# Optimization experiments

Hardware: AMD Instinct MI355X
Metric: run time of the kernel (lower is better)

Reference implementation:

```python
import jax, jax.numpy as jnp
import numpy as np

TOP_K = 2


def setup_inputs() -> dict:
    key = jax.random.key(0)
    k1, k2, k3, k4 = jax.random.split(key, 4)
    B, T, D = 1, 2048, 1024
    E, F = 8, 2048
    scale_in = 1.0 / np.sqrt(D)
    scale_f = 1.0 / np.sqrt(F)
    x = jax.random.normal(k1, (B, T, D), dtype=jnp.float32)
    Wr = jax.random.normal(k2, (E, D), dtype=jnp.float32) * scale_in  # router weight [E, D]
    W1 = jax.random.normal(k3, (E, F, D), dtype=jnp.float32) * scale_in  # fc1 weights stacked [E, F, D]
    W2 = jax.random.normal(k4, (E, D, F), dtype=jnp.float32) * scale_f  # fc2 weights stacked [E, D, F]
    return {"x": x, "Wr": Wr, "W1": W1, "W2": W2}


def reference(x, Wr, W1, W2):
    B, T, D = x.shape
    E = Wr.shape[0]
    xf = x.reshape(B * T, D)  # [N, D]
    N = xf.shape[0]

    # Router: softmax over experts, top-k gating, renormalized
    logits = xf @ Wr.T  # [N, E]
    probs = jax.nn.softmax(logits, axis=-1)
    top_vals, top_idx = jax.lax.top_k(probs, TOP_K)  # [N, K]
    top_vals = top_vals / jnp.sum(top_vals, axis=-1, keepdims=True)

    # Dense per-token gate matrix: gates[n, e] = sum_k top_vals[n,k] * (top_idx[n,k]==e)
    gates = jnp.zeros((N, E), dtype=x.dtype).at[
        jnp.arange(N)[:, None], top_idx
    ].add(top_vals)  # [N, E]

    # Expert MLP: fc2(relu(fc1(x))^2), computed densely for all experts then
    # combined with the (mostly-zero) gate weights.
    h = jnp.einsum("nd,efd->nef", xf, W1)  # [N, E, F]
    a = jnp.square(jax.nn.relu(h))
    y = jnp.einsum("nef,edf->ned", a, W2)  # [N, E, D]
    out = jnp.einsum("ne,ned->nd", gates, y)  # [N, D]
    return out.reshape(B, T, D)
```

## Files before the change

kernel.cpp:

```cpp
#include <hip/hip_runtime.h>
#include <hip/hip_bf16.h>
#include <cstdint>
#include <cstddef>

#define N_TOK 2048
#define DIM   1024
#define NEXP  8
#define FDIM  2048

#define BM 128
#define BN 128
#define BK 64

typedef __attribute__((ext_vector_type(8))) short short8;
typedef __attribute__((ext_vector_type(4))) float f32x4;
typedef unsigned short ushort_t;

#define OFF_COUNTS  0
#define OFF_TOK     4096
#define OFF_GATE    (OFF_TOK + NEXP * N_TOK * 4)
#define OFF_A       ((size_t)1 << 20)
#define OFF_W1B     (OFF_A  + (size_t)2 * N_TOK * FDIM * 2)
#define OFF_W2B     (OFF_W1B + (size_t)NEXP * FDIM * DIM * 2)
#define OFF_XB      (OFF_W2B + (size_t)NEXP * DIM * FDIM * 2)

__device__ __forceinline__ uint32_t cvt2(float lo, float hi) {
  __hip_bfloat162 p = __float22bfloat162_rn(make_float2(lo, hi));
  uint32_t r; __builtin_memcpy(&r, &p, 4); return r;
}

__device__ __forceinline__ void gl16(const ushort_t* g, const ushort_t* l) {
  __builtin_amdgcn_global_load_lds(
      (const __attribute__((address_space(1))) void*)g,
      (__attribute__((address_space(3))) void*)l, 16, 0, 0);
}

#define W1_U8 ((size_t)NEXP * FDIM * DIM / 8)
#define W2_U8 W1_U8
#define X_U8  ((size_t)N_TOK * DIM / 8)
__global__ __launch_bounds__(256) void prep_kernel(
    const float* __restrict__ W1, const float* __restrict__ W2, const float* __restrict__ x,
    ushort_t* __restrict__ W1b, ushort_t* __restrict__ W2b, ushort_t* __restrict__ xb) {
  size_t stride = (size_t)gridDim.x * 256;
  for (size_t u = (size_t)blockIdx.x * 256 + threadIdx.x; u < W1_U8 + W2_U8 + X_U8; u += stride) {
    const float* s; ushort_t* d; size_t o;
    if (u < W1_U8)              { s = W1; d = W1b; o = u; }
    else if (u < W1_U8 + W2_U8) { s = W2; d = W2b; o = u - W1_U8; }
    else                        { s = x;  d = xb;  o = u - W1_U8 - W2_U8; }
    float4 a = *(const float4*)(s + o * 8);
    float4 b = *(const float4*)(s + o * 8 + 4);
    *(uint4*)(d + o * 8) = make_uint4(cvt2(a.x, a.y), cvt2(a.z, a.w), cvt2(b.x, b.y), cvt2(b.z, b.w));
  }
}

__global__ __launch_bounds__(64) void router_kernel(
    const float* __restrict__ x, const float* __restrict__ Wr,
    int* __restrict__ counts, int* __restrict__ toklist,
    float* __restrict__ gatelist) {
  int n = blockIdx.x;
  int lane = threadIdx.x;
  const float* xr = x + (size_t)n * DIM;

  float xv[DIM / 64];
#pragma unroll
  for (int i = 0; i < DIM / 64; ++i) xv[i] = xr[lane + 64 * i];

  float logit[NEXP];
#pragma unroll
  for (int e = 0; e < NEXP; ++e) {
    const float* wr = Wr + (size_t)e * DIM;
    float s = 0.f;
#pragma unroll
    for (int i = 0; i < DIM / 64; ++i) s += xv[i] * wr[lane + 64 * i];
#pragma unroll
    for (int off = 32; off; off >>= 1) s += __shfl_down(s, off);
    logit[e] = s;
  }

  if (lane == 0) {
    float m = logit[0];
#pragma unroll
    for (int e = 1; e < NEXP; ++e) m = fmaxf(m, logit[e]);
    float p[NEXP];
#pragma unroll
    for (int e = 0; e < NEXP; ++e) p[e] = expf(logit[e] - m);
    int i1 = 0;
#pragma unroll
    for (int e = 1; e < NEXP; ++e) if (p[e] > p[i1]) i1 = e;
    int i2 = (i1 == 0) ? 1 : 0;
#pragma unroll
    for (int e = 0; e < NEXP; ++e)
      if (e != i1 && p[e] > p[i2]) i2 = e;
    float denom = p[i1] + p[i2];

    int pos1 = atomicAdd(&counts[i1], 1);
    toklist[i1 * N_TOK + pos1] = n;
    gatelist[i1 * N_TOK + pos1] = p[i1] / denom;

    int pos2 = atomicAdd(&counts[i2], 1);
    toklist[i2 * N_TOK + pos2] = n;
    gatelist[i2 * N_TOK + pos2] = p[i2] / denom;
  }
}

__global__ __launch_bounds__(256, 3) void fc1_mfma(
    const ushort_t* __restrict__ xb, const ushort_t* __restrict__ W1b,
    const int* __restrict__ counts, const int* __restrict__ toklist,
    __hip_bfloat16* __restrict__ Abuf) {
  const int ROWB = N_TOK / BM;
  const int COLB = FDIM / BN;
  int bid = blockIdx.x;
  int e  = bid / (ROWB * COLB);
  int rb = (bid / COLB) % ROWB;
  int cb = bid % COLB;
  int ne = counts[e];
  if (rb * BM >= ne) return;
  int base = 0;
  for (int i = 0; i < e; ++i) base += counts[i];

  __shared__ ushort_t As[BM * BK];
  __shared__ ushort_t Bs[BN * BK];

  int tid = threadIdx.x, lane = tid & 63, w = tid >> 6;

  const ushort_t* gA[4]; const ushort_t* gB[4];
  const ushort_t* lA[4]; const ushort_t* lB[4];
#pragma unroll
  for (int i = 0; i < 4; ++i) {
    int row = w * 32 + i * 8 + (lane >> 3);
    int c16 = (lane & 7) ^ (row & 7);
    int r = rb * BM + row; if (r >= ne) r = ne - 1;
    int tok = toklist[e * N_TOK + r];
    gA[i] = xb + (size_t)tok * DIM + c16 * 8;
    gB[i] = W1b + ((size_t)e * FDIM + cb * BN + row) * DIM + c16 * 8;
    lA[i] = &As[w * 2048 + i * 512];
    lB[i] = &Bs[w * 2048 + i * 512];
  }

  int wr = (w >> 1) * 64, wc = (w & 1) * 64;
  int lr = lane & 15, lg = lane >> 4;
  f32x4 acc[4][4] = {};

  for (int t = 0; t < DIM / BK; ++t) {
    __syncthreads();
#pragma unroll
    for (int i = 0; i < 4; ++i) {
      gl16(gA[i], lA[i]); gl16(gB[i], lB[i]);
      gA[i] += BK; gB[i] += BK;
    }
    __syncthreads();
#pragma unroll
    for (int ks = 0; ks < 2; ++ks) {
      short8 af[4], bf[4];
#pragma unroll
      for (int m = 0; m < 4; ++m) {
        int row = wr + m * 16 + lr;
        af[m] = *(const short8*)&As[row * BK + (((ks * 4 + lg) ^ (row & 7)) * 8)];
      }
#pragma unroll
      for (int n = 0; n < 4; ++n) {
        int row = wc + n * 16 + lr;
        bf[n] = *(const short8*)&Bs[row * BK + (((ks * 4 + lg) ^ (row & 7)) * 8)];
      }
#pragma unroll
      for (int m = 0; m < 4; ++m)
#pragma unroll
        for (int n = 0; n < 4; ++n)
          acc[m][n] = __builtin_amdgcn_mfma_f32_16x16x32_bf16(af[m], bf[n], acc[m][n], 0, 0, 0);
    }
  }

  int colbase = cb * BN + wc + lr;
#pragma unroll
  for (int m = 0; m < 4; ++m) {
#pragma unroll
    for (int j = 0; j < 4; ++j) {
      int r = rb * BM + wr + m * 16 + lg * 4 + j;
      if (r < ne) {
        __hip_bfloat16* orow = Abuf + (size_t)(base + r) * FDIM + colbase;
#pragma unroll
        for (int n = 0; n < 4; ++n) {
          float v = fmaxf(acc[m][n][j], 0.f);
          orow[n * 16] = __float2bfloat16(v * v);
        }
      }
    }
  }
}

__global__ __launch_bounds__(256, 3) void fc2_mfma(
    const ushort_t* __restrict__ Abuf, const ushort_t* __restrict__ W2b,
    const int* __restrict__ counts, const int* __restrict__ toklist,
    const float* __restrict__ gatelist, float* __restrict__ out) {
  const int ROWB = N_TOK / BM;
  const int COLB = DIM / BN;
  int bid = blockIdx.x;
  int e  = bid / (ROWB * COLB);
  int rb = (bid / COLB) % ROWB;
  int cb = bid % COLB;
  int ks0 = blockIdx.y * (FDIM / 2);
  int ne = counts[e];
  if (rb * BM >= ne) return;
  int base = 0;
  for (int i = 0; i < e; ++i) base += counts[i];

  __shared__ ushort_t As[BM * BK];
  __shared__ ushort_t Bs[BN * BK];

  int tid = threadIdx.x, lane = tid & 63, w = tid >> 6;

  const ushort_t* gA[4]; const ushort_t* gB[4];
  const ushort_t* lA[4]; const ushort_t* lB[4];
#pragma unroll
  for (int i = 0; i < 4; ++i) {
    int row = w * 32 + i * 8 + (lane >> 3);
    int c16 = (lane & 7) ^ (row & 7);
    int r = rb * BM + row; if (r >= ne) r = ne - 1;
    gA[i] = Abuf + (size_t)(base + r) * FDIM + ks0 + c16 * 8;
    gB[i] = W2b + ((size_t)e * DIM + cb * BN + row) * FDIM + ks0 + c16 * 8;
    lA[i] = &As[w * 2048 + i * 512];
    lB[i] = &Bs[w * 2048 + i * 512];
  }

  int wr = (w >> 1) * 64, wc = (w & 1) * 64;
  int lr = lane & 15, lg = lane >> 4;
  f32x4 acc[4][4] = {};

  for (int t = 0; t < (FDIM / 2) / BK; ++t) {
    __syncthreads();
#pragma unroll
    for (int i = 0; i < 4; ++i) {
      gl16(gA[i], lA[i]); gl16(gB[i], lB[i]);
      gA[i] += BK; gB[i] += BK;
    }
    __syncthreads();
#pragma unroll
    for (int ks = 0; ks < 2; ++ks) {
      short8 af[4], bf[4];
#pragma unroll
      for (int m = 0; m < 4; ++m) {
        int row = wr + m * 16 + lr;
        af[m] = *(const short8*)&As[row * BK + (((ks * 4 + lg) ^ (row & 7)) * 8)];
      }
#pragma unroll
      for (int n = 0; n < 4; ++n) {
        int row = wc + n * 16 + lr;
        bf[n] = *(const short8*)&Bs[row * BK + (((ks * 4 + lg) ^ (row & 7)) * 8)];
      }
#pragma unroll
      for (int m = 0; m < 4; ++m)
#pragma unroll
        for (int n = 0; n < 4; ++n)
          acc[m][n] = __builtin_amdgcn_mfma_f32_16x16x32_bf16(af[m], bf[n], acc[m][n], 0, 0, 0);
    }
  }

  int colbase = cb * BN + wc + lr;
#pragma unroll
  for (int m = 0; m < 4; ++m) {
#pragma unroll
    for (int j = 0; j < 4; ++j) {
      int r = rb * BM + wr + m * 16 + lg * 4 + j;
      if (r < ne) {
        int tok = toklist[e * N_TOK + r];
        float g = gatelist[e * N_TOK + r];
        float* orow = out + (size_t)tok * DIM + colbase;
#pragma unroll
        for (int n = 0; n < 4; ++n)
          atomicAdd(&orow[n * 16], g * acc[m][n][j]);
      }
    }
  }
}

extern "C" void kernel_launch(void* const* d_in, const int* in_sizes, int n_in,
                              void* d_out, int out_size, void* d_ws, size_t ws_size,
                              hipStream_t stream) {
  const float* x  = (const float*)d_in[0];
  const float* Wr = (const float*)d_in[1];
  const float* W1 = (const float*)d_in[2];
  const float* W2 = (const float*)d_in[3];
  float* out = (float*)d_out;

  char* ws = (char*)d_ws;
  int*   counts   = (int*)(ws + OFF_COUNTS);
  int*   toklist  = (int*)(ws + OFF_TOK);
  float* gatelist = (float*)(ws + OFF_GATE);
  __hip_bfloat16* Abuf = (__hip_bfloat16*)(ws + OFF_A);
  ushort_t* W1b = (ushort_t*)(ws + OFF_W1B);
  ushort_t* W2b = (ushort_t*)(ws + OFF_W2B);
  ushort_t* xb  = (ushort_t*)(ws + OFF_XB);

  (void)hipMemsetAsync(counts, 0, NEXP * sizeof(int), stream);
  (void)hipMemsetAsync(out, 0, (size_t)out_size * sizeof(float), stream);

  prep_kernel<<<4096, 256, 0, stream>>>(W1, W2, x, W1b, W2b, xb);

  router_kernel<<<N_TOK, 64, 0, stream>>>(x, Wr, counts, toklist, gatelist);

  fc1_mfma<<<NEXP * (N_TOK / BM) * (FDIM / BN), 256, 0, stream>>>(
      xb, W1b, counts, toklist, Abuf);

  fc2_mfma<<<dim3(NEXP * (N_TOK / BM) * (DIM / BN), 2), 256, 0, stream>>>(
      (const ushort_t*)Abuf, W2b, counts, toklist, gatelist, out);
}
```

Measured before the change: 293.9 us.

## Restructure prep conversion, batch router tokens per block, add XCD-aware block swizzle

The fp32-to-bf16 prep kernel changes from a grid-stride loop with per-element branching to fixed 16384-element chunks per block, with an unrolled 8-step loop. The router now handles four tokens per 256-thread block instead of one token per 64-thread block, which cuts the block count. The fc1 and fc2 GEMM kernels remap block IDs so consecutive logical tiles land on the same XCD, aiming for better L2 reuse of expert weights. The prep chunking hardcodes sizes that must divide the tensor shapes exactly.

```diff
diff --git a/kernel.cpp b/kernel.cpp
--- a/kernel.cpp
+++ b/kernel.cpp
@@ -35,30 +35,38 @@
       (__attribute__((address_space(3))) void*)l, 16, 0, 0);
 }
 
-#define W1_U8 ((size_t)NEXP * FDIM * DIM / 8)
-#define W2_U8 W1_U8
-#define X_U8  ((size_t)N_TOK * DIM / 8)
+__device__ __forceinline__ int xcd_swz(int bid, int nwg) {
+  int q = nwg >> 3, r = nwg & 7;
+  int xcd = bid & 7, local = bid >> 3;
+  int base = (xcd < r) ? xcd * (q + 1) : r * (q + 1) + (xcd - r) * q;
+  return base + local;
+}
+
 __global__ __launch_bounds__(256) void prep_kernel(
     const float* __restrict__ W1, const float* __restrict__ W2, const float* __restrict__ x,
     ushort_t* __restrict__ W1b, ushort_t* __restrict__ W2b, ushort_t* __restrict__ xb) {
-  size_t stride = (size_t)gridDim.x * 256;
-  for (size_t u = (size_t)blockIdx.x * 256 + threadIdx.x; u < W1_U8 + W2_U8 + X_U8; u += stride) {
-    const float* s; ushort_t* d; size_t o;
-    if (u < W1_U8)              { s = W1; d = W1b; o = u; }
-    else if (u < W1_U8 + W2_U8) { s = W2; d = W2b; o = u - W1_U8; }
-    else                        { s = x;  d = xb;  o = u - W1_U8 - W2_U8; }
-    float4 a = *(const float4*)(s + o * 8);
-    float4 b = *(const float4*)(s + o * 8 + 4);
-    *(uint4*)(d + o * 8) = make_uint4(cvt2(a.x, a.y), cvt2(a.z, a.w), cvt2(b.x, b.y), cvt2(b.z, b.w));
-  }
-}
-
-__global__ __launch_bounds__(64) void router_kernel(
+  int b = blockIdx.x;
+  const float* s; ushort_t* d; size_t off;
+  if (b < 1024)      { s = W1; d = W1b; off = (size_t)b * 16384; }
+  else if (b < 2048) { s = W2; d = W2b; off = (size_t)(b - 1024) * 16384; }
+  else               { s = x;  d = xb;  off = (size_t)(b - 2048) * 16384; }
+  s += off; d += off;
+  int t8 = threadIdx.x * 8;
+#pragma unroll
+  for (int j = 0; j < 8; ++j) {
+    float4 f0 = *(const float4*)(s + j * 2048 + t8);
+    float4 f1 = *(const float4*)(s + j * 2048 + t8 + 4);
+    *(uint4*)(d + j * 2048 + t8) =
+        make_uint4(cvt2(f0.x, f0.y), cvt2(f0.z, f0.w), cvt2(f1.x, f1.y), cvt2(f1.z, f1.w));
+  }
+}
+
+__global__ __launch_bounds__(256) void router_kernel(
     const float* __restrict__ x, const float* __restrict__ Wr,
     int* __restrict__ counts, int* __restrict__ toklist,
     float* __restrict__ gatelist) {
-  int n = blockIdx.x;
-  int lane = threadIdx.x;
+  int n = blockIdx.x * 4 + (threadIdx.x >> 6);
+  int lane = threadIdx.x & 63;
   const float* xr = x + (size_t)n * DIM;
 
   float xv[DIM / 64];
@@ -109,7 +117,7 @@
     __hip_bfloat16* __restrict__ Abuf) {
   const int ROWB = N_TOK / BM;
   const int COLB = FDIM / BN;
-  int bid = blockIdx.x;
+  int bid = xcd_swz(blockIdx.x, NEXP * ROWB * COLB);
   int e  = bid / (ROWB * COLB);
   int rb = (bid / COLB) % ROWB;
   int cb = bid % COLB;
@@ -194,7 +202,7 @@
     const float* __restrict__ gatelist, float* __restrict__ out) {
   const int ROWB = N_TOK / BM;
   const int COLB = DIM / BN;
-  int bid = blockIdx.x;
+  int bid = xcd_swz(blockIdx.x, NEXP * ROWB * COLB);
   int e  = bid / (ROWB * COLB);
   int rb = (bid / COLB) % ROWB;
   int cb = bid % COLB;
@@ -294,9 +302,9 @@
   (void)hipMemsetAsync(counts, 0, NEXP * sizeof(int), stream);
   (void)hipMemsetAsync(out, 0, (size_t)out_size * sizeof(float), stream);
 
-  prep_kernel<<<4096, 256, 0, stream>>>(W1, W2, x, W1b, W2b, xb);
-
-  router_kernel<<<N_TOK, 64, 0, stream>>>(x, Wr, counts, toklist, gatelist);
+  prep_kernel<<<2176, 256, 0, stream>>>(W1, W2, x, W1b, W2b, xb);
+
+  router_kernel<<<N_TOK / 4, 256, 0, stream>>>(x, Wr, counts, toklist, gatelist);
 
   fc1_mfma<<<NEXP * (N_TOK / BM) * (FDIM / BN), 256, 0, stream>>>(
       xb, W1b, counts, toklist, Abuf);
```

Result: no change. 295.5 us (+0.6%).
